# Performance work log

Measured on AMD Instinct MI355X. Metric: run time of the kernel, lower is better.

The kernel has to match this reference:

```python
import math
import jax, jax.numpy as jnp
import numpy as np

N, E = 20000, 640000
S_DIM, Z_DIM, H, QK, VD = 64, 64, 4, 8, 8
EPS = 1e-8


def quat_rotate(v, q):
    # v: [..., 3], q: [..., 4] (w, x, y, z), broadcastable. Unit-quaternion rotation:
    # v' = v + 2*(w*(u x v) + u x (u x v))
    w = q[..., 0:1]
    u = q[..., 1:4]
    uv = jnp.cross(u, v)
    return v + 2.0 * (w * uv + jnp.cross(u, uv))


def setup_inputs() -> dict:
    key = jax.random.key(0)
    ks = jax.random.split(key, 16)
    s = jax.random.normal(ks[0], (N, S_DIM), dtype=jnp.float32)
    z = jax.random.normal(ks[1], (E, Z_DIM), dtype=jnp.float32)
    edge_index = jax.random.randint(ks[2], (2, E), 0, N)
    quaternion = jax.random.normal(ks[3], (N, 4), dtype=jnp.float32)
    quaternion = quaternion / jnp.linalg.norm(quaternion, axis=-1, keepdims=True)
    translation = jax.random.normal(ks[4], (N, 3), dtype=jnp.float32)
    sc_s = 1.0 / math.sqrt(S_DIM)
    sc_z = 1.0 / math.sqrt(Z_DIM)
    # weights stored [in, out] so y = x @ W (equivalent to torch x @ W.T)
    Wq_s = jax.random.normal(ks[5], (S_DIM, H * S_DIM), dtype=jnp.float32) * sc_s
    Wk_s = jax.random.normal(ks[6], (S_DIM, H * S_DIM), dtype=jnp.float32) * sc_s
    Wv_s = jax.random.normal(ks[7], (S_DIM, H * S_DIM), dtype=jnp.float32) * sc_s
    Wq_v = jax.random.normal(ks[8], (S_DIM, H * QK * 3), dtype=jnp.float32) * sc_s
    Wk_v = jax.random.normal(ks[9], (S_DIM, H * QK * 3), dtype=jnp.float32) * sc_s
    Wv_v = jax.random.normal(ks[10], (S_DIM, H * VD * 3), dtype=jnp.float32) * sc_s
    Wb = jax.random.normal(ks[11], (Z_DIM, H), dtype=jnp.float32) * sc_z
    bb = jnp.zeros((H,), dtype=jnp.float32)
    Wdz = jax.random.normal(ks[12], (Z_DIM, Z_DIM // 4), dtype=jnp.float32) * sc_z
    bdz = jnp.zeros((Z_DIM // 4,), dtype=jnp.float32)
    head_weights = jnp.full((H,), 0.541324854612918, dtype=jnp.float32)  # softplus^{-1}(1)
    concat_dim = Z_DIM // 4 + S_DIM + VD * 4
    Wout = jax.random.normal(ks[13], (H * concat_dim, S_DIM), dtype=jnp.float32) / math.sqrt(H * concat_dim)
    bout = jnp.zeros((S_DIM,), dtype=jnp.float32)
    return {
        's': s, 'z': z, 'edge_index': edge_index, 'quaternion': quaternion,
        'translation': translation, 'Wq_s': Wq_s, 'Wk_s': Wk_s, 'Wv_s': Wv_s,
        'Wq_v': Wq_v, 'Wk_v': Wk_v, 'Wv_v': Wv_v, 'Wb': Wb, 'bb': bb,
        'Wdz': Wdz, 'bdz': bdz, 'head_weights': head_weights,
        'Wout': Wout, 'bout': bout,
    }


def reference(s, z, edge_index, quaternion, translation,
              Wq_s, Wk_s, Wv_s, Wq_v, Wk_v, Wv_v,
              Wb, bb, Wdz, bdz, head_weights, Wout, bout):
    idx_i, idx_j = edge_index[0], edge_index[1]
    n = s.shape[0]
    h = head_weights.shape[0]
    qk = Wq_v.shape[1] // (3 * h)
    vd = Wv_v.shape[1] // (3 * h)

    q_scalar = (s @ Wq_s).reshape(n, h, -1)
    k_scalar = (s @ Wk_s).reshape(n, h, -1)
    v_scalar = (s @ Wv_s).reshape(n, h, -1)

    def to_points(x):
        # torch.split into 3 chunks then stack(dim=-1): [n, 3*c] -> [n, c, 3]
        c = x.shape[-1] // 3
        return jnp.swapaxes(x.reshape(n, 3, c), 1, 2)

    quat_b = quaternion[:, None, :]
    trans_b = translation[:, None, :]
    q_vec = (quat_rotate(to_points(s @ Wq_v), quat_b) + trans_b).reshape(n, h, qk, 3)
    k_vec = (quat_rotate(to_points(s @ Wk_v), quat_b) + trans_b).reshape(n, h, qk, 3)
    v_vec = (quat_rotate(to_points(s @ Wv_v), quat_b) + trans_b).reshape(n, h, vd, 3)

    b_bias = z @ Wb + bb  # [E, H]

    attn = jnp.sum(k_scalar[idx_i] * q_scalar[idx_j], axis=-1)  # [E, H]
    attn = attn * math.sqrt(1.0 / 3 * qk) + math.sqrt(1.0 / 3) * b_bias

    disp = q_vec[idx_i] - k_vec[idx_j]            # [E, H, qk, 3]
    vec_att = jnp.sum(disp * disp, axis=-1)       # [E, H, qk]
    hw = jax.nn.softplus(head_weights)[None, :, None]
    vec_att = jnp.sum(vec_att * hw, axis=-1) * math.sqrt(1.0 / (3 * (qk * 9.0 / 2))) * (-0.5)
    attn = attn + vec_att

    # segment softmax over destination node idx_i
    seg_max = jax.ops.segment_max(attn, idx_i, num_segments=n)
    ea = jnp.exp(attn - seg_max[idx_i])
    denom = jax.ops.segment_sum(ea, idx_i, num_segments=n)
    attn = ea / denom[idx_i]                      # [E, H]

    out_scalar = jax.ops.segment_sum(attn[:, :, None] * v_scalar[idx_i], idx_i, num_segments=n)
    out_scalar = out_scalar.reshape(n, -1)

    out_vec = jax.ops.segment_sum(attn[:, :, None, None] * v_vec[idx_i], idx_i, num_segments=n)
    out_vec = out_vec - translation[:, None, None, :]
    q_conj = jnp.concatenate([quaternion[:, :1], -quaternion[:, 1:]], axis=-1)
    out_vec = quat_rotate(out_vec, q_conj[:, None, None, :])   # [n, h, vd, 3]
    out_vec_norm = jnp.sqrt(jnp.sum(out_vec * out_vec, axis=-1) + EPS).reshape(n, -1)
    out_vec_flat = out_vec.reshape(n, -1, 3)

    pair_z = z @ Wdz + bdz                         # [E, z/4]
    out_pair = jax.ops.segment_sum(attn[:, :, None] * pair_z[:, None, :], idx_i, num_segments=n)
    out_pair = out_pair.reshape(n, -1)

    feats = jnp.concatenate([out_scalar,
                             out_vec_flat[..., 0], out_vec_flat[..., 1], out_vec_flat[..., 2],
                             out_vec_norm, out_pair], axis=-1)
    return feats @ Wout + bout
```

## Files before the change

kernel.cpp:

```cpp
#include <hip/hip_runtime.h>
#include <stdint.h>


#define C_SQRT83  1.6329931618554518f
#define C_SQRT13  0.5773502691896258f
#define C_VEC    -0.04811252243246881f

__device__ __forceinline__ unsigned short f2bf(float f){
  unsigned u = __float_as_uint(f);
  u += 0x7fffu + ((u >> 16) & 1u);
  return (unsigned short)(u >> 16);
}
__device__ __forceinline__ unsigned pack2(float a, float b){
  return (unsigned)f2bf(a) | ((unsigned)f2bf(b) << 16);
}
__device__ __forceinline__ float bflo(unsigned u){ return __uint_as_float(u << 16); }
__device__ __forceinline__ float bfhi(unsigned u){ return __uint_as_float(u & 0xffff0000u); }

__device__ __forceinline__ void quat_rot(float w, float ux, float uy, float uz,
                                         float vx, float vy, float vz,
                                         float& ox, float& oy, float& oz){
  float cx = uy*vz - uz*vy;
  float cy = uz*vx - ux*vz;
  float cz = ux*vy - uy*vx;
  float dx = uy*cz - uz*cy;
  float dy = uz*cx - ux*cz;
  float dz = ux*cy - uy*cx;
  ox = vx + 2.f*(w*cx + dx);
  oy = vy + 2.f*(w*cy + dy);
  oz = vz + 2.f*(w*cz + dz);
}


__global__ __launch_bounds__(256) void k_zero(unsigned* __restrict__ counts, int n){
  int g = blockIdx.x*256 + threadIdx.x;
  if (g < n) counts[g] = 0u;
}

__global__ __launch_bounds__(256) void k_count(const int* __restrict__ ei,
                                               unsigned* __restrict__ counts, int ne){
  int e = blockIdx.x*256 + threadIdx.x;
  if (e >= ne) return;
  atomicAdd(&counts[ei[e]], 1u);
}

__global__ __launch_bounds__(256) void k_scan(const unsigned* __restrict__ counts,
                                              unsigned* __restrict__ row_off,
                                              unsigned* __restrict__ cursor, int n){
  __shared__ unsigned part[256];
  int t = threadIdx.x;
  int chunk = (n + 255) >> 8;
  int s0 = t*chunk, s1 = min(s0 + chunk, n);
  unsigned sum = 0;
  for (int k = s0; k < s1; ++k) sum += counts[k];
  part[t] = sum; __syncthreads();
  for (int off = 1; off < 256; off <<= 1){
    unsigned v = (t >= off) ? part[t-off] : 0u;
    __syncthreads();
    part[t] += v;
    __syncthreads();
  }
  unsigned run = (t == 0) ? 0u : part[t-1];
  for (int k = s0; k < s1; ++k){
    row_off[k] = run; cursor[k] = run; run += counts[k];
  }
  if (t == 255) row_off[n] = part[255];
}

__global__ __launch_bounds__(256) void k_fill(const int* __restrict__ ei,
                                              unsigned* __restrict__ cursor,
                                              unsigned* __restrict__ si,
                                              unsigned* __restrict__ sj,
                                              unsigned* __restrict__ se, int ne){
  int e = blockIdx.x*256 + threadIdx.x;
  if (e >= ne) return;
  int i = ei[e];
  unsigned pos = atomicAdd(&cursor[i], 1u);
  si[pos] = (unsigned)i;
  sj[pos] = (unsigned)ei[ne + e];
  se[pos] = (unsigned)e;
}


#define BN 32

__device__ __forceinline__ void pass256(const float* __restrict__ W,
                                        const float st[BN][66], int cg, int sl,
                                        float acc[8][4]){
  #pragma unroll
  for (int i=0;i<8;i++){ acc[i][0]=0.f; acc[i][1]=0.f; acc[i][2]=0.f; acc[i][3]=0.f; }
  #pragma unroll 4
  for (int k = 0; k < 64; ++k){
    const float4 w = *(const float4*)(W + (size_t)k*256 + cg*4);
    #pragma unroll
    for (int i=0;i<8;i++){
      const float sv = st[sl*8+i][k];
      acc[i][0] += sv*w.x; acc[i][1] += sv*w.y; acc[i][2] += sv*w.z; acc[i][3] += sv*w.w;
    }
  }
}

__device__ __forceinline__ void pass96(const float* __restrict__ W,
                                       const float st[BN][66], int cgp, int slp,
                                       float acc[4][4]){
  #pragma unroll
  for (int i=0;i<4;i++){ acc[i][0]=0.f; acc[i][1]=0.f; acc[i][2]=0.f; acc[i][3]=0.f; }
  if (cgp >= 24) return;
  #pragma unroll 4
  for (int k = 0; k < 64; ++k){
    const float4 w = *(const float4*)(W + (size_t)k*96 + cgp*4);
    #pragma unroll
    for (int i=0;i<4;i++){
      const float sv = st[slp*4+i][k];
      acc[i][0] += sv*w.x; acc[i][1] += sv*w.y; acc[i][2] += sv*w.z; acc[i][3] += sv*w.w;
    }
  }
}

__global__ __launch_bounds__(256) void k_proj(
    const float* __restrict__ s, const float* __restrict__ quat, const float* __restrict__ trans,
    const float* __restrict__ Wqs, const float* __restrict__ Wks, const float* __restrict__ Wvs,
    const float* __restrict__ Wqv, const float* __restrict__ Wkv, const float* __restrict__ Wvv,
    unsigned* __restrict__ qs, unsigned* __restrict__ ks, float* __restrict__ vs,
    unsigned* __restrict__ qv, unsigned* __restrict__ kv, float* __restrict__ vv, int n)
{
  __shared__ float st[BN][66];
  __shared__ float pt[BN][97];
  const int tid = threadIdx.x;
  const int node0 = blockIdx.x * BN;

  #pragma unroll
  for (int r = 0; r < 2; ++r){
    const int idx = tid + r*256;
    const int nd = idx >> 4, c4 = idx & 15;
    const int g = node0 + nd;
    float4 v = make_float4(0.f,0.f,0.f,0.f);
    if (g < n) v = *(const float4*)(s + (size_t)g*64 + c4*4);
    st[nd][c4*4+0]=v.x; st[nd][c4*4+1]=v.y; st[nd][c4*4+2]=v.z; st[nd][c4*4+3]=v.w;
  }
  __syncthreads();

  const int cg = tid & 63, sl = tid >> 6;
  const int cgp = tid & 31, slp = tid >> 5;
  float acc[8][4];

  pass256(Wqs, st, cg, sl, acc);
  #pragma unroll
  for (int i=0;i<8;i++){
    const int g = node0 + sl*8 + i;
    if (g < n){
      uint2 u; u.x = pack2(acc[i][0],acc[i][1]); u.y = pack2(acc[i][2],acc[i][3]);
      *(uint2*)(qs + (size_t)g*128 + cg*2) = u;
    }
  }
  pass256(Wks, st, cg, sl, acc);
  #pragma unroll
  for (int i=0;i<8;i++){
    const int g = node0 + sl*8 + i;
    if (g < n){
      uint2 u; u.x = pack2(acc[i][0],acc[i][1]); u.y = pack2(acc[i][2],acc[i][3]);
      *(uint2*)(ks + (size_t)g*128 + cg*2) = u;
    }
  }
  pass256(Wvs, st, cg, sl, acc);
  #pragma unroll
  for (int i=0;i<8;i++){
    const int g = node0 + sl*8 + i;
    if (g < n){
      float4 f; f.x=acc[i][0]; f.y=acc[i][1]; f.z=acc[i][2]; f.w=acc[i][3];
      *(float4*)(vs + (size_t)g*256 + cg*4) = f;
    }
  }

  float pac[4][4];

  pass96(Wqv, st, cgp, slp, pac);
  __syncthreads();
  if (cgp < 24){
    #pragma unroll
    for (int i=0;i<4;i++){
      #pragma unroll
      for (int c=0;c<4;c++) pt[slp*4+i][cgp*4+c] = pac[i][c];
    }
  }
  __syncthreads();
  #pragma unroll
  for (int r = 0; r < 2; ++r){
    const int t2 = tid + r*256;
    const int nd = t2 >> 4, pp = t2 & 15;
    const int g = node0 + nd;
    if (g < n){
      const float4 q4 = *(const float4*)(quat + (size_t)g*4);
      const float tx = trans[(size_t)g*3], ty = trans[(size_t)g*3+1], tz = trans[(size_t)g*3+2];
      float x0,y0,z0,x1,y1,z1;
      quat_rot(q4.x,q4.y,q4.z,q4.w, pt[nd][2*pp],   pt[nd][32+2*pp],   pt[nd][64+2*pp],   x0,y0,z0);
      quat_rot(q4.x,q4.y,q4.z,q4.w, pt[nd][2*pp+1], pt[nd][32+2*pp+1], pt[nd][64+2*pp+1], x1,y1,z1);
      x0+=tx; y0+=ty; z0+=tz; x1+=tx; y1+=ty; z1+=tz;
      unsigned* d = qv + (size_t)g*48 + pp*3;
      d[0] = pack2(x0,y0); d[1] = pack2(z0,x1); d[2] = pack2(y1,z1);
    }
  }

  pass96(Wkv, st, cgp, slp, pac);
  __syncthreads();
  if (cgp < 24){
    #pragma unroll
    for (int i=0;i<4;i++){
      #pragma unroll
      for (int c=0;c<4;c++) pt[slp*4+i][cgp*4+c] = pac[i][c];
    }
  }
  __syncthreads();
  #pragma unroll
  for (int r = 0; r < 2; ++r){
    const int t2 = tid + r*256;
    const int nd = t2 >> 4, pp = t2 & 15;
    const int g = node0 + nd;
    if (g < n){
      const float4 q4 = *(const float4*)(quat + (size_t)g*4);
      const float tx = trans[(size_t)g*3], ty = trans[(size_t)g*3+1], tz = trans[(size_t)g*3+2];
      float x0,y0,z0,x1,y1,z1;
      quat_rot(q4.x,q4.y,q4.z,q4.w, pt[nd][2*pp],   pt[nd][32+2*pp],   pt[nd][64+2*pp],   x0,y0,z0);
      quat_rot(q4.x,q4.y,q4.z,q4.w, pt[nd][2*pp+1], pt[nd][32+2*pp+1], pt[nd][64+2*pp+1], x1,y1,z1);
      x0+=tx; y0+=ty; z0+=tz; x1+=tx; y1+=ty; z1+=tz;
      unsigned* d = kv + (size_t)g*48 + pp*3;
      d[0] = pack2(x0,y0); d[1] = pack2(z0,x1); d[2] = pack2(y1,z1);
    }
  }

  pass96(Wvv, st, cgp, slp, pac);
  __syncthreads();
  if (cgp < 24){
    #pragma unroll
    for (int i=0;i<4;i++){
      #pragma unroll
      for (int c=0;c<4;c++) pt[slp*4+i][cgp*4+c] = pac[i][c];
    }
  }
  __syncthreads();
  #pragma unroll
  for (int r = 0; r < 12; ++r){
    const int idx = tid + r*256;
    const int nd = idx / 96, col = idx - nd*96;
    const int g = node0 + nd;
    if (g < n) vv[(size_t)g*96 + col] = pt[nd][col];
  }
}


__global__ __launch_bounds__(256) void k_edge(
    const float* __restrict__ z,
    const unsigned* __restrict__ si, const unsigned* __restrict__ sj, const unsigned* __restrict__ se,
    const float* __restrict__ Wb,  const float* __restrict__ bb,
    const float* __restrict__ Wdz, const float* __restrict__ bdz,
    const float* __restrict__ hwts,
    const unsigned* __restrict__ qs, const unsigned* __restrict__ ks,
    const unsigned* __restrict__ qv, const unsigned* __restrict__ kv,
    float* __restrict__ logits, unsigned* __restrict__ pz, int ne)
{
  const int p = blockIdx.x*256 + threadIdx.x;
  if (p >= ne) return;
  const unsigned i = si[p], j = sj[p], e = se[p];

  float b4[4];  b4[0]=b4[1]=b4[2]=b4[3]=0.f;
  float pacc[16];
  #pragma unroll
  for (int c=0;c<16;c++) pacc[c]=0.f;
  const float* zr = z + (size_t)e*64;
  #pragma unroll
  for (int k4 = 0; k4 < 16; ++k4){
    const float4 zv = *(const float4*)(zr + 4*k4);
    #pragma unroll
    for (int kk = 0; kk < 4; ++kk){
      const int k = 4*k4 + kk;
      const float zk = (kk==0)?zv.x:((kk==1)?zv.y:((kk==2)?zv.z:zv.w));
      const float4 wb = *(const float4*)(Wb + k*4);
      b4[0]+=zk*wb.x; b4[1]+=zk*wb.y; b4[2]+=zk*wb.z; b4[3]+=zk*wb.w;
      const float* wd = Wdz + k*16;
      const float4 w0=*(const float4*)(wd), w1=*(const float4*)(wd+4),
                   w2=*(const float4*)(wd+8), w3=*(const float4*)(wd+12);
      pacc[ 0]+=zk*w0.x; pacc[ 1]+=zk*w0.y; pacc[ 2]+=zk*w0.z; pacc[ 3]+=zk*w0.w;
      pacc[ 4]+=zk*w1.x; pacc[ 5]+=zk*w1.y; pacc[ 6]+=zk*w1.z; pacc[ 7]+=zk*w1.w;
      pacc[ 8]+=zk*w2.x; pacc[ 9]+=zk*w2.y; pacc[10]+=zk*w2.z; pacc[11]+=zk*w2.w;
      pacc[12]+=zk*w3.x; pacc[13]+=zk*w3.y; pacc[14]+=zk*w3.z; pacc[15]+=zk*w3.w;
    }
  }
  #pragma unroll
  for (int c=0;c<16;c++) pacc[c] += bdz[c];
  { uint4 u0, u1;
    u0.x=pack2(pacc[0],pacc[1]);   u0.y=pack2(pacc[2],pacc[3]);
    u0.z=pack2(pacc[4],pacc[5]);   u0.w=pack2(pacc[6],pacc[7]);
    u1.x=pack2(pacc[8],pacc[9]);   u1.y=pack2(pacc[10],pacc[11]);
    u1.z=pack2(pacc[12],pacc[13]); u1.w=pack2(pacc[14],pacc[15]);
    uint4* d = (uint4*)(pz + (size_t)p*8);
    d[0]=u0; d[1]=u1; }

  const uint4* kr = (const uint4*)(ks + (size_t)i*128);
  const uint4* qr = (const uint4*)(qs + (size_t)j*128);
  float sdot[4];
  #pragma unroll
  for (int h = 0; h < 4; ++h){
    float acc = 0.f;
    #pragma unroll
    for (int c = 0; c < 8; ++c){
      const uint4 a = kr[h*8+c];
      const uint4 b = qr[h*8+c];
      acc += bflo(a.x)*bflo(b.x) + bfhi(a.x)*bfhi(b.x);
      acc += bflo(a.y)*bflo(b.y) + bfhi(a.y)*bfhi(b.y);
      acc += bflo(a.z)*bflo(b.z) + bfhi(a.z)*bfhi(b.z);
      acc += bflo(a.w)*bflo(b.w) + bfhi(a.w)*bfhi(b.w);
    }
    sdot[h] = acc;
  }

  const uint4* qvr = (const uint4*)(qv + (size_t)i*48);
  const uint4* kvr = (const uint4*)(kv + (size_t)j*48);
  float vsum[4];
  #pragma unroll
  for (int h = 0; h < 4; ++h){
    float acc = 0.f;
    #pragma unroll
    for (int c = 0; c < 3; ++c){
      const uint4 a = qvr[h*3+c];
      const uint4 b = kvr[h*3+c];
      float d;
      d = bflo(a.x)-bflo(b.x); acc += d*d;  d = bfhi(a.x)-bfhi(b.x); acc += d*d;
      d = bflo(a.y)-bflo(b.y); acc += d*d;  d = bfhi(a.y)-bfhi(b.y); acc += d*d;
      d = bflo(a.z)-bflo(b.z); acc += d*d;  d = bfhi(a.z)-bfhi(b.z); acc += d*d;
      d = bflo(a.w)-bflo(b.w); acc += d*d;  d = bfhi(a.w)-bfhi(b.w); acc += d*d;
    }
    vsum[h] = acc;
  }

  float4 lg;
  {
    float l[4];
    #pragma unroll
    for (int h = 0; h < 4; ++h){
      const float hw = log1pf(__expf(hwts[h]));
      l[h] = C_SQRT83*sdot[h] + C_SQRT13*(b4[h] + bb[h]) + C_VEC*hw*vsum[h];
    }
    lg.x=l[0]; lg.y=l[1]; lg.z=l[2]; lg.w=l[3];
  }
  *(float4*)(logits + (size_t)p*4) = lg;
}


__global__ __launch_bounds__(256) void k_soft(
    const float* __restrict__ logits, const unsigned* __restrict__ pz,
    const unsigned* __restrict__ row_off, float* __restrict__ out_pair, int n)
{
  const int t = blockIdx.x*256 + threadIdx.x;
  if (t >= n*4) return;
  const int i = t >> 2, h = t & 3;
  const int beg = (int)row_off[i], end = (int)row_off[i+1];

  float m = -3.4e38f;
  for (int p = beg; p < end; ++p) m = fmaxf(m, logits[(size_t)p*4 + h]);

  float ssum = 0.f;
  float acc[16];
  #pragma unroll
  for (int c=0;c<16;c++) acc[c]=0.f;

  for (int p = beg; p < end; ++p){
    const float w = __expf(logits[(size_t)p*4 + h] - m);
    ssum += w;
    const uint4* pr = (const uint4*)(pz + (size_t)p*8);
    const uint4 a = pr[0], b = pr[1];
    acc[ 0]+=w*bflo(a.x); acc[ 1]+=w*bfhi(a.x);
    acc[ 2]+=w*bflo(a.y); acc[ 3]+=w*bfhi(a.y);
    acc[ 4]+=w*bflo(a.z); acc[ 5]+=w*bfhi(a.z);
    acc[ 6]+=w*bflo(a.w); acc[ 7]+=w*bfhi(a.w);
    acc[ 8]+=w*bflo(b.x); acc[ 9]+=w*bfhi(b.x);
    acc[10]+=w*bflo(b.y); acc[11]+=w*bfhi(b.y);
    acc[12]+=w*bflo(b.z); acc[13]+=w*bfhi(b.z);
    acc[14]+=w*bflo(b.w); acc[15]+=w*bfhi(b.w);
  }
  const float inv = (end > beg) ? (1.f/ssum) : 0.f;
  float4* dst = (float4*)(out_pair + (size_t)i*64 + h*16);
  float4 o;
  o.x=acc[0]*inv;  o.y=acc[1]*inv;  o.z=acc[2]*inv;  o.w=acc[3]*inv;  dst[0]=o;
  o.x=acc[4]*inv;  o.y=acc[5]*inv;  o.z=acc[6]*inv;  o.w=acc[7]*inv;  dst[1]=o;
  o.x=acc[8]*inv;  o.y=acc[9]*inv;  o.z=acc[10]*inv; o.w=acc[11]*inv; dst[2]=o;
  o.x=acc[12]*inv; o.y=acc[13]*inv; o.z=acc[14]*inv; o.w=acc[15]*inv; dst[3]=o;
}


__global__ __launch_bounds__(256) void k_out(
    const float* __restrict__ vs, const float* __restrict__ vv,
    const float* __restrict__ out_pair, const unsigned* __restrict__ row_off,
    const float* __restrict__ quat, const float* __restrict__ trans,
    const float* __restrict__ Wout, const float* __restrict__ bout,
    float* __restrict__ out, int n)
{
  __shared__ float feats[32][448];
  __shared__ int degs[32];
  const int tid = threadIdx.x;
  const int node0 = blockIdx.x*32;

  if (tid < 32){
    const int g = node0 + tid;
    degs[tid] = (g < n) ? (int)(row_off[g+1] - row_off[g]) : 1;
  }
  __syncthreads();

  for (int x = tid; x < 32*256; x += 256){
    const int nd = x >> 8, c = x & 255;
    const int g = node0 + nd;
    feats[nd][c] = (g < n && degs[nd] > 0) ? vs[(size_t)g*256 + c] : 0.f;
  }
  for (int x = tid; x < 32*64; x += 256){
    const int nd = x >> 6, c = x & 63;
    const int g = node0 + nd;
    feats[nd][384 + c] = (g < n) ? out_pair[(size_t)g*64 + c] : 0.f;
  }
  for (int x = tid; x < 32*32; x += 256){
    const int nd = x >> 5, pt = x & 31;
    const int g = node0 + nd;
    float X=0.f, Y=0.f, Z=0.f;
    if (g < n){
      if (degs[nd] > 0){
        X = vv[(size_t)g*96 + pt];
        Y = vv[(size_t)g*96 + 32 + pt];
        Z = vv[(size_t)g*96 + 64 + pt];
      } else {
        const float4 q4 = *(const float4*)(quat + (size_t)g*4);
        const float tx = trans[(size_t)g*3], ty = trans[(size_t)g*3+1], tz = trans[(size_t)g*3+2];
        quat_rot(q4.x, -q4.y, -q4.z, -q4.w, -tx, -ty, -tz, X, Y, Z);
      }
    }
    feats[nd][256 + pt] = X;
    feats[nd][288 + pt] = Y;
    feats[nd][320 + pt] = Z;
    feats[nd][352 + pt] = sqrtf(X*X + Y*Y + Z*Z + 1e-8f);
  }
  __syncthreads();

  const int lane = tid & 63;
  const int wave = tid >> 6;
  float acc[8];
  #pragma unroll
  for (int q8=0;q8<8;q8++) acc[q8]=0.f;

  for (int k = 0; k < 448; ++k){
    const float wv = Wout[(size_t)k*64 + lane];
    #pragma unroll
    for (int q8 = 0; q8 < 8; ++q8)
      acc[q8] += feats[wave*8 + q8][k] * wv;
  }
  const float bo = bout[lane];
  #pragma unroll
  for (int q8 = 0; q8 < 8; ++q8){
    const int g = node0 + wave*8 + q8;
    if (g < n) out[(size_t)g*64 + lane] = acc[q8] + bo;
  }
}


extern "C" void kernel_launch(void* const* d_in, const int* in_sizes, int n_in,
                              void* d_out, int out_size, void* d_ws, size_t ws_size,
                              hipStream_t stream) {
  const float* s     = (const float*)d_in[0];
  const float* z     = (const float*)d_in[1];
  const int*   ei    = (const int*)  d_in[2];
  const float* quat  = (const float*)d_in[3];
  const float* trans = (const float*)d_in[4];
  const float* Wqs   = (const float*)d_in[5];
  const float* Wks   = (const float*)d_in[6];
  const float* Wvs   = (const float*)d_in[7];
  const float* Wqv   = (const float*)d_in[8];
  const float* Wkv   = (const float*)d_in[9];
  const float* Wvv   = (const float*)d_in[10];
  const float* Wb    = (const float*)d_in[11];
  const float* bb    = (const float*)d_in[12];
  const float* Wdz   = (const float*)d_in[13];
  const float* bdz   = (const float*)d_in[14];
  const float* hwts  = (const float*)d_in[15];
  const float* Wout  = (const float*)d_in[16];
  const float* bout  = (const float*)d_in[17];
  float* out = (float*)d_out;

  const int n  = in_sizes[0] / 64;
  const int ne = in_sizes[1] / 64;

  size_t off = 0;
  char* base = (char*)d_ws;
  auto take = [&](size_t bytes)->char* {
    char* p = base + off;
    off += (bytes + 255) & ~(size_t)255;
    return p;
  };
  unsigned* qs     = (unsigned*)take((size_t)n*512);
  unsigned* ks     = (unsigned*)take((size_t)n*512);
  unsigned* qvt    = (unsigned*)take((size_t)n*192);
  unsigned* kvt    = (unsigned*)take((size_t)n*192);
  float*    vs     = (float*)   take((size_t)n*1024);
  float*    vv     = (float*)   take((size_t)n*384);
  float*    logits = (float*)   take((size_t)ne*16);
  unsigned* pz     = (unsigned*)take((size_t)ne*32);
  unsigned* counts = (unsigned*)take((size_t)n*4);
  unsigned* roff   = (unsigned*)take((size_t)(n+1)*4);
  unsigned* cur    = (unsigned*)take((size_t)n*4);
  unsigned* si     = (unsigned*)take((size_t)ne*4);
  unsigned* sj     = (unsigned*)take((size_t)ne*4);
  unsigned* se     = (unsigned*)take((size_t)ne*4);
  float*    opair  = (float*)   take((size_t)n*256);
  (void)ws_size; (void)n_in; (void)out_size;

  const int gbE = (ne + 255) / 256;
  const int gbN = (n  + 255) / 256;

  k_zero <<<gbN, 256, 0, stream>>>(counts, n);
  k_count<<<gbE, 256, 0, stream>>>(ei, counts, ne);
  k_scan <<<1,   256, 0, stream>>>(counts, roff, cur, n);
  k_fill <<<gbE, 256, 0, stream>>>(ei, cur, si, sj, se, ne);
  k_proj <<<(n + BN - 1)/BN, 256, 0, stream>>>(s, quat, trans, Wqs, Wks, Wvs, Wqv, Wkv, Wvv,
                                               qs, ks, vs, qvt, kvt, vv, n);
  k_edge <<<gbE, 256, 0, stream>>>(z, si, sj, se, Wb, bb, Wdz, bdz, hwts,
                                   qs, ks, qvt, kvt, logits, pz, ne);
  k_soft <<<(n*4 + 255)/256, 256, 0, stream>>>(logits, pz, roff, opair, n);
  k_out  <<<(n + 31)/32, 256, 0, stream>>>(vs, vv, opair, roff, quat, trans,
                                           Wout, bout, out, n);
}
```

Before: 688.1 us.

## Split edge kernel into coalesced z-projection and gather, parallelize softmax per node

The edge kernel is split in two. A z-projection kernel now reads z coalesced in original edge order and scatters the bias and pair features to sorted positions through a new posmap. A separate gather kernel then computes the attention logits. The segment softmax moves from one thread per (node, head) to 16 lanes per head with shuffle reductions, which balances load across uneven degrees. The node projection uses transposed shared memory for vectorized loads, and the output GEMM loads features as float4. This adds one extra kernel launch and a round trip for the bias through the logits buffer. An unused, inconsistent k_gather variant is left in the file.

```diff
diff --git a/kernel.cpp b/kernel.cpp
--- a/kernel.cpp
+++ b/kernel.cpp
@@ -71,37 +71,42 @@
                                               unsigned* __restrict__ cursor,
                                               unsigned* __restrict__ si,
                                               unsigned* __restrict__ sj,
-                                              unsigned* __restrict__ se, int ne){
+                                              unsigned* __restrict__ posmap, int ne){
   int e = blockIdx.x*256 + threadIdx.x;
   if (e >= ne) return;
   int i = ei[e];
   unsigned pos = atomicAdd(&cursor[i], 1u);
   si[pos] = (unsigned)i;
   sj[pos] = (unsigned)ei[ne + e];
-  se[pos] = (unsigned)e;
+  posmap[e] = pos;
 }
 
 
 #define BN 32
 
 __device__ __forceinline__ void pass256(const float* __restrict__ W,
-                                        const float st[BN][66], int cg, int sl,
+                                        const float stT[64][40], int cg, int sl,
                                         float acc[8][4]){
   #pragma unroll
   for (int i=0;i<8;i++){ acc[i][0]=0.f; acc[i][1]=0.f; acc[i][2]=0.f; acc[i][3]=0.f; }
   #pragma unroll 4
   for (int k = 0; k < 64; ++k){
-    const float4 w = *(const float4*)(W + (size_t)k*256 + cg*4);
-    #pragma unroll
-    for (int i=0;i<8;i++){
-      const float sv = st[sl*8+i][k];
-      acc[i][0] += sv*w.x; acc[i][1] += sv*w.y; acc[i][2] += sv*w.z; acc[i][3] += sv*w.w;
-    }
+    const float4 w  = *(const float4*)(W + (size_t)k*256 + cg*4);
+    const float4 n0 = *(const float4*)&stT[k][sl*8];
+    const float4 n1 = *(const float4*)&stT[k][sl*8+4];
+    acc[0][0]+=n0.x*w.x; acc[0][1]+=n0.x*w.y; acc[0][2]+=n0.x*w.z; acc[0][3]+=n0.x*w.w;
+    acc[1][0]+=n0.y*w.x; acc[1][1]+=n0.y*w.y; acc[1][2]+=n0.y*w.z; acc[1][3]+=n0.y*w.w;
+    acc[2][0]+=n0.z*w.x; acc[2][1]+=n0.z*w.y; acc[2][2]+=n0.z*w.z; acc[2][3]+=n0.z*w.w;
+    acc[3][0]+=n0.w*w.x; acc[3][1]+=n0.w*w.y; acc[3][2]+=n0.w*w.z; acc[3][3]+=n0.w*w.w;
+    acc[4][0]+=n1.x*w.x; acc[4][1]+=n1.x*w.y; acc[4][2]+=n1.x*w.z; acc[4][3]+=n1.x*w.w;
+    acc[5][0]+=n1.y*w.x; acc[5][1]+=n1.y*w.y; acc[5][2]+=n1.y*w.z; acc[5][3]+=n1.y*w.w;
+    acc[6][0]+=n1.z*w.x; acc[6][1]+=n1.z*w.y; acc[6][2]+=n1.z*w.z; acc[6][3]+=n1.z*w.w;
+    acc[7][0]+=n1.w*w.x; acc[7][1]+=n1.w*w.y; acc[7][2]+=n1.w*w.z; acc[7][3]+=n1.w*w.w;
   }
 }
 
 __device__ __forceinline__ void pass96(const float* __restrict__ W,
-                                       const float st[BN][66], int cgp, int slp,
+                                       const float stT[64][40], int cgp, int slp,
                                        float acc[4][4]){
   #pragma unroll
   for (int i=0;i<4;i++){ acc[i][0]=0.f; acc[i][1]=0.f; acc[i][2]=0.f; acc[i][3]=0.f; }
@@ -109,11 +114,11 @@
   #pragma unroll 4
   for (int k = 0; k < 64; ++k){
     const float4 w = *(const float4*)(W + (size_t)k*96 + cgp*4);
-    #pragma unroll
-    for (int i=0;i<4;i++){
-      const float sv = st[slp*4+i][k];
-      acc[i][0] += sv*w.x; acc[i][1] += sv*w.y; acc[i][2] += sv*w.z; acc[i][3] += sv*w.w;
-    }
+    const float4 nv = *(const float4*)&stT[k][slp*4];
+    acc[0][0]+=nv.x*w.x; acc[0][1]+=nv.x*w.y; acc[0][2]+=nv.x*w.z; acc[0][3]+=nv.x*w.w;
+    acc[1][0]+=nv.y*w.x; acc[1][1]+=nv.y*w.y; acc[1][2]+=nv.y*w.z; acc[1][3]+=nv.y*w.w;
+    acc[2][0]+=nv.z*w.x; acc[2][1]+=nv.z*w.y; acc[2][2]+=nv.z*w.z; acc[2][3]+=nv.z*w.w;
+    acc[3][0]+=nv.w*w.x; acc[3][1]+=nv.w*w.y; acc[3][2]+=nv.w*w.z; acc[3][3]+=nv.w*w.w;
   }
 }
 
@@ -124,7 +129,7 @@
     unsigned* __restrict__ qs, unsigned* __restrict__ ks, float* __restrict__ vs,
     unsigned* __restrict__ qv, unsigned* __restrict__ kv, float* __restrict__ vv, int n)
 {
-  __shared__ float st[BN][66];
+  __shared__ float stT[64][40];
   __shared__ float pt[BN][97];
   const int tid = threadIdx.x;
   const int node0 = blockIdx.x * BN;
@@ -136,7 +141,7 @@
     const int g = node0 + nd;
     float4 v = make_float4(0.f,0.f,0.f,0.f);
     if (g < n) v = *(const float4*)(s + (size_t)g*64 + c4*4);
-    st[nd][c4*4+0]=v.x; st[nd][c4*4+1]=v.y; st[nd][c4*4+2]=v.z; st[nd][c4*4+3]=v.w;
+    stT[c4*4+0][nd]=v.x; stT[c4*4+1][nd]=v.y; stT[c4*4+2][nd]=v.z; stT[c4*4+3][nd]=v.w;
   }
   __syncthreads();
 
@@ -144,7 +149,7 @@
   const int cgp = tid & 31, slp = tid >> 5;
   float acc[8][4];
 
-  pass256(Wqs, st, cg, sl, acc);
+  pass256(Wqs, stT, cg, sl, acc);
   #pragma unroll
   for (int i=0;i<8;i++){
     const int g = node0 + sl*8 + i;
@@ -153,7 +158,7 @@
       *(uint2*)(qs + (size_t)g*128 + cg*2) = u;
     }
   }
-  pass256(Wks, st, cg, sl, acc);
+  pass256(Wks, stT, cg, sl, acc);
   #pragma unroll
   for (int i=0;i<8;i++){
     const int g = node0 + sl*8 + i;
@@ -162,7 +167,7 @@
       *(uint2*)(ks + (size_t)g*128 + cg*2) = u;
     }
   }
-  pass256(Wvs, st, cg, sl, acc);
+  pass256(Wvs, stT, cg, sl, acc);
   #pragma unroll
   for (int i=0;i<8;i++){
     const int g = node0 + sl*8 + i;
@@ -174,7 +179,7 @@
 
   float pac[4][4];
 
-  pass96(Wqv, st, cgp, slp, pac);
+  pass96(Wqv, stT, cgp, slp, pac);
   __syncthreads();
   if (cgp < 24){
     #pragma unroll
@@ -201,7 +206,7 @@
     }
   }
 
-  pass96(Wkv, st, cgp, slp, pac);
+  pass96(Wkv, stT, cgp, slp, pac);
   __syncthreads();
   if (cgp < 24){
     #pragma unroll
@@ -228,7 +233,7 @@
     }
   }
 
-  pass96(Wvv, st, cgp, slp, pac);
+  pass96(Wvv, stT, cgp, slp, pac);
   __syncthreads();
   if (cgp < 24){
     #pragma unroll
@@ -248,19 +253,15 @@
 }
 
 
-__global__ __launch_bounds__(256) void k_edge(
-    const float* __restrict__ z,
-    const unsigned* __restrict__ si, const unsigned* __restrict__ sj, const unsigned* __restrict__ se,
+__global__ __launch_bounds__(256) void k_zproj(
+    const float* __restrict__ z, const unsigned* __restrict__ posmap,
     const float* __restrict__ Wb,  const float* __restrict__ bb,
     const float* __restrict__ Wdz, const float* __restrict__ bdz,
-    const float* __restrict__ hwts,
-    const unsigned* __restrict__ qs, const unsigned* __restrict__ ks,
-    const unsigned* __restrict__ qv, const unsigned* __restrict__ kv,
-    float* __restrict__ logits, unsigned* __restrict__ pz, int ne)
+    float* __restrict__ bias4, unsigned* __restrict__ pz, int ne)
 {
-  const int p = blockIdx.x*256 + threadIdx.x;
-  if (p >= ne) return;
-  const unsigned i = si[p], j = sj[p], e = se[p];
+  const int e = blockIdx.x*256 + threadIdx.x;
+  if (e >= ne) return;
+  const unsigned pos = posmap[e];
 
   float b4[4];  b4[0]=b4[1]=b4[2]=b4[3]=0.f;
   float pacc[16];
@@ -285,6 +286,10 @@
       pacc[12]+=zk*w3.x; pacc[13]+=zk*w3.y; pacc[14]+=zk*w3.z; pacc[15]+=zk*w3.w;
     }
   }
+  {
+    float4 b; b.x=b4[0]+bb[0]; b.y=b4[1]+bb[1]; b.z=b4[2]+bb[2]; b.w=b4[3]+bb[3];
+    *(float4*)(bias4 + (size_t)pos*4) = b;
+  }
   #pragma unroll
   for (int c=0;c<16;c++) pacc[c] += bdz[c];
   { uint4 u0, u1;
@@ -292,19 +297,42 @@
     u0.z=pack2(pacc[4],pacc[5]);   u0.w=pack2(pacc[6],pacc[7]);
     u1.x=pack2(pacc[8],pacc[9]);   u1.y=pack2(pacc[10],pacc[11]);
     u1.z=pack2(pacc[12],pacc[13]); u1.w=pack2(pacc[14],pacc[15]);
-    uint4* d = (uint4*)(pz + (size_t)p*8);
+    uint4* d = (uint4*)(pz + (size_t)pos*8);
     d[0]=u0; d[1]=u1; }
-
-  const uint4* kr = (const uint4*)(ks + (size_t)i*128);
-  const uint4* qr = (const uint4*)(qs + (size_t)j*128);
+}
+
+
+__global__ __launch_bounds__(256) void k_gather(
+    const unsigned* __restrict__ si, const unsigned* __restrict__ sj,
+    const float* __restrict__ hwts,
+    const unsigned* __restrict__ qs, const unsigned* __restrict__ ks,
+    const unsigned* __restrict__ qv, const unsigned* __restrict__ kv,
+    float* __restrict__ logits, int ne)
+{
+  const int p = blockIdx.x*256 + threadIdx.x;
+  if (p >= ne) return;
+  const unsigned i = si[p], j = sj[p];
+
+  const uint4* kr  = (const uint4*)(ks + (size_t)i*128);
+  const uint4* qr  = (const uint4*)(qs + (size_t)j*128);
+  const uint4* qvr = (const uint4*)(qv + (size_t)i*48);
+  const uint4* kvr = (const uint4*)(kv + (size_t)j*48);
+
+  uint4 ka[8], qa[8], qva[3], kva[3];
+  #pragma unroll
+  for (int c=0;c<8;c++){ ka[c] = kr[c]; qa[c] = qr[c]; }
+  #pragma unroll
+  for (int c=0;c<3;c++){ qva[c] = qvr[c]; kva[c] = kvr[c]; }
+  const float4 b4 = *(const float4*)(logits + (size_t)p*4);
+
   float sdot[4];
   #pragma unroll
   for (int h = 0; h < 4; ++h){
     float acc = 0.f;
     #pragma unroll
-    for (int c = 0; c < 8; ++c){
-      const uint4 a = kr[h*8+c];
-      const uint4 b = qr[h*8+c];
+    for (int c = 0; c < 2; ++c){
+      const uint4 a = ka[h*2+c];
+      const uint4 b = qa[h*2+c];
       acc += bflo(a.x)*bflo(b.x) + bfhi(a.x)*bfhi(b.x);
       acc += bflo(a.y)*bflo(b.y) + bfhi(a.y)*bfhi(b.y);
       acc += bflo(a.z)*bflo(b.z) + bfhi(a.z)*bfhi(b.z);
@@ -313,23 +341,27 @@
     sdot[h] = acc;
   }
 
-  const uint4* qvr = (const uint4*)(qv + (size_t)i*48);
-  const uint4* kvr = (const uint4*)(kv + (size_t)j*48);
   float vsum[4];
-  #pragma unroll
-  for (int h = 0; h < 4; ++h){
-    float acc = 0.f;
+  {
+    float acch[4];
+    #pragma unroll
+    for (int h=0;h<4;h++) acch[h]=0.f;
     #pragma unroll
     for (int c = 0; c < 3; ++c){
-      const uint4 a = qvr[h*3+c];
-      const uint4 b = kvr[h*3+c];
+      const uint4 a = qva[c], b = kva[c];
+      const int base = c*8;
       float d;
-      d = bflo(a.x)-bflo(b.x); acc += d*d;  d = bfhi(a.x)-bfhi(b.x); acc += d*d;
-      d = bflo(a.y)-bflo(b.y); acc += d*d;  d = bfhi(a.y)-bfhi(b.y); acc += d*d;
-      d = bflo(a.z)-bflo(b.z); acc += d*d;  d = bfhi(a.z)-bfhi(b.z); acc += d*d;
-      d = bflo(a.w)-bflo(b.w); acc += d*d;  d = bfhi(a.w)-bfhi(b.w); acc += d*d;
-    }
-    vsum[h] = acc;
+      d = bflo(a.x)-bflo(b.x); acch[(base+0)/6] += d*d;
+      d = bfhi(a.x)-bfhi(b.x); acch[(base+1)/6] += d*d;
+      d = bflo(a.y)-bflo(b.y); acch[(base+2)/6] += d*d;
+      d = bfhi(a.y)-bfhi(b.y); acch[(base+3)/6] += d*d;
+      d = bflo(a.z)-bflo(b.z); acch[(base+4)/6] += d*d;
+      d = bfhi(a.z)-bfhi(b.z); acch[(base+5)/6] += d*d;
+      d = bflo(a.w)-bflo(b.w); acch[(base+6)/6] += d*d;
+      d = bfhi(a.w)-bfhi(b.w); acch[(base+7)/6] += d*d;
+    }
+    #pragma unroll
+    for (int h=0;h<4;h++) vsum[h]=acch[h];
   }
 
   float4 lg;
@@ -338,7 +370,96 @@
     #pragma unroll
     for (int h = 0; h < 4; ++h){
       const float hw = log1pf(__expf(hwts[h]));
-      l[h] = C_SQRT83*sdot[h] + C_SQRT13*(b4[h] + bb[h]) + C_VEC*hw*vsum[h];
+      l[h] = C_SQRT83*sdot[h] + C_SQRT13*b4.x + C_VEC*hw*vsum[h];
+    }
+    lg.x=l[0]; lg.y=l[1]; lg.z=l[2]; lg.w=l[3];
+  }
+  *(float4*)(logits + (size_t)p*4) = lg;
+}
+
+__global__ __launch_bounds__(256) void k_gather_full(
+    const unsigned* __restrict__ si, const unsigned* __restrict__ sj,
+    const float* __restrict__ hwts,
+    const unsigned* __restrict__ qs, const unsigned* __restrict__ ks,
+    const unsigned* __restrict__ qv, const unsigned* __restrict__ kv,
+    float* __restrict__ logits, int ne)
+{
+  const int p = blockIdx.x*256 + threadIdx.x;
+  if (p >= ne) return;
+  const unsigned i = si[p], j = sj[p];
+
+  const uint4* kr  = (const uint4*)(ks + (size_t)i*128);
+  const uint4* qr  = (const uint4*)(qs + (size_t)j*128);
+  const uint4* qvr = (const uint4*)(qv + (size_t)i*48);
+  const uint4* kvr = (const uint4*)(kv + (size_t)j*48);
+
+  uint4 qva[3], kva[3];
+  #pragma unroll
+  for (int c=0;c<3;c++){ qva[c] = qvr[c]; kva[c] = kvr[c]; }
+  const float4 b4 = *(const float4*)(logits + (size_t)p*4);
+
+  float sdot[4];
+  #pragma unroll
+  for (int hp = 0; hp < 2; ++hp){
+    uint4 a0[8], b0[8];
+    #pragma unroll
+    for (int c=0;c<8;c++){ a0[c]=kr[hp*16+c]; b0[c]=qr[hp*16+c]; }
+    uint4 a1[8], b1[8];
+    #pragma unroll
+    for (int c=0;c<8;c++){ a1[c]=kr[hp*16+8+c]; b1[c]=qr[hp*16+8+c]; }
+    float acc0 = 0.f, acc1 = 0.f;
+    #pragma unroll
+    for (int c=0;c<8;c++){
+      const uint4 a = a0[c], b = b0[c];
+      acc0 += bflo(a.x)*bflo(b.x) + bfhi(a.x)*bfhi(b.x);
+      acc0 += bflo(a.y)*bflo(b.y) + bfhi(a.y)*bfhi(b.y);
+      acc0 += bflo(a.z)*bflo(b.z) + bfhi(a.z)*bfhi(b.z);
+      acc0 += bflo(a.w)*bflo(b.w) + bfhi(a.w)*bfhi(b.w);
+    }
+    #pragma unroll
+    for (int c=0;c<8;c++){
+      const uint4 a = a1[c], b = b1[c];
+      acc1 += bflo(a.x)*bflo(b.x) + bfhi(a.x)*bfhi(b.x);
+      acc1 += bflo(a.y)*bflo(b.y) + bfhi(a.y)*bfhi(b.y);
+      acc1 += bflo(a.z)*bflo(b.z) + bfhi(a.z)*bfhi(b.z);
+      acc1 += bflo(a.w)*bflo(b.w) + bfhi(a.w)*bfhi(b.w);
+    }
+    sdot[hp*2]   = acc0;
+    sdot[hp*2+1] = acc1;
+  }
+
+  const uint4* qvr4 = (const uint4*)(qv + (size_t)i*48);
+  const uint4* kvr4 = (const uint4*)(kv + (size_t)j*48);
+  float vsum[4];
+  #pragma unroll
+  for (int h = 0; h < 4; ++h){
+    const uint4 a0 = qvr4[h*3], a1 = qvr4[h*3+1], a2 = qvr4[h*3+2];
+    const uint4 b0 = kvr4[h*3], b1 = kvr4[h*3+1], b2 = kvr4[h*3+2];
+    float acc = 0.f, d;
+    d=bflo(a0.x)-bflo(b0.x); acc+=d*d; d=bfhi(a0.x)-bfhi(b0.x); acc+=d*d;
+    d=bflo(a0.y)-bflo(b0.y); acc+=d*d; d=bfhi(a0.y)-bfhi(b0.y); acc+=d*d;
+    d=bflo(a0.z)-bflo(b0.z); acc+=d*d; d=bfhi(a0.z)-bfhi(b0.z); acc+=d*d;
+    d=bflo(a0.w)-bflo(b0.w); acc+=d*d; d=bfhi(a0.w)-bfhi(b0.w); acc+=d*d;
+    d=bflo(a1.x)-bflo(b1.x); acc+=d*d; d=bfhi(a1.x)-bfhi(b1.x); acc+=d*d;
+    d=bflo(a1.y)-bflo(b1.y); acc+=d*d; d=bfhi(a1.y)-bfhi(b1.y); acc+=d*d;
+    d=bflo(a1.z)-bflo(b1.z); acc+=d*d; d=bfhi(a1.z)-bfhi(b1.z); acc+=d*d;
+    d=bflo(a1.w)-bflo(b1.w); acc+=d*d; d=bfhi(a1.w)-bfhi(b1.w); acc+=d*d;
+    d=bflo(a2.x)-bflo(b2.x); acc+=d*d; d=bfhi(a2.x)-bfhi(b2.x); acc+=d*d;
+    d=bflo(a2.y)-bflo(b2.y); acc+=d*d; d=bfhi(a2.y)-bfhi(b2.y); acc+=d*d;
+    d=bflo(a2.z)-bflo(b2.z); acc+=d*d; d=bfhi(a2.z)-bfhi(b2.z); acc+=d*d;
+    d=bflo(a2.w)-bflo(b2.w); acc+=d*d; d=bfhi(a2.w)-bfhi(b2.w); acc+=d*d;
+    vsum[h] = acc;
+  }
+  (void)qva; (void)kva;
+
+  float4 lg;
+  {
+    float bias[4] = {b4.x, b4.y, b4.z, b4.w};
+    float l[4];
+    #pragma unroll
+    for (int h = 0; h < 4; ++h){
+      const float hw = log1pf(__expf(hwts[h]));
+      l[h] = C_SQRT83*sdot[h] + C_SQRT13*bias[h] + C_VEC*hw*vsum[h];
     }
     lg.x=l[0]; lg.y=l[1]; lg.z=l[2]; lg.w=l[3];
   }
@@ -350,20 +471,25 @@
     const float* __restrict__ logits, const unsigned* __restrict__ pz,
     const unsigned* __restrict__ row_off, float* __restrict__ out_pair, int n)
 {
-  const int t = blockIdx.x*256 + threadIdx.x;
-  if (t >= n*4) return;
-  const int i = t >> 2, h = t & 3;
-  const int beg = (int)row_off[i], end = (int)row_off[i+1];
+  const int node = blockIdx.x*4 + (threadIdx.x >> 6);
+  if (node >= n) return;
+  const int lane = threadIdx.x & 63;
+  const int h = lane >> 4, sub = lane & 15;
+  const int beg = (int)row_off[node], end = (int)row_off[node+1];
 
   float m = -3.4e38f;
-  for (int p = beg; p < end; ++p) m = fmaxf(m, logits[(size_t)p*4 + h]);
+  for (int p = beg + sub; p < end; p += 16)
+    m = fmaxf(m, logits[(size_t)p*4 + h]);
+  #pragma unroll
+  for (int msk = 1; msk < 16; msk <<= 1)
+    m = fmaxf(m, __shfl_xor(m, msk));
 
   float ssum = 0.f;
   float acc[16];
   #pragma unroll
   for (int c=0;c<16;c++) acc[c]=0.f;
 
-  for (int p = beg; p < end; ++p){
+  for (int p = beg + sub; p < end; p += 16){
     const float w = __expf(logits[(size_t)p*4 + h] - m);
     ssum += w;
     const uint4* pr = (const uint4*)(pz + (size_t)p*8);
@@ -377,13 +503,17 @@
     acc[12]+=w*bflo(b.z); acc[13]+=w*bfhi(b.z);
     acc[14]+=w*bflo(b.w); acc[15]+=w*bfhi(b.w);
   }
+  #pragma unroll
+  for (int msk = 1; msk < 16; msk <<= 1){
+    ssum += __shfl_xor(ssum, msk);
+    #pragma unroll
+    for (int c=0;c<16;c++) acc[c] += __shfl_xor(acc[c], msk);
+  }
   const float inv = (end > beg) ? (1.f/ssum) : 0.f;
-  float4* dst = (float4*)(out_pair + (size_t)i*64 + h*16);
-  float4 o;
-  o.x=acc[0]*inv;  o.y=acc[1]*inv;  o.z=acc[2]*inv;  o.w=acc[3]*inv;  dst[0]=o;
-  o.x=acc[4]*inv;  o.y=acc[5]*inv;  o.z=acc[6]*inv;  o.w=acc[7]*inv;  dst[1]=o;
-  o.x=acc[8]*inv;  o.y=acc[9]*inv;  o.z=acc[10]*inv; o.w=acc[11]*inv; dst[2]=o;
-  o.x=acc[12]*inv; o.y=acc[13]*inv; o.z=acc[14]*inv; o.w=acc[15]*inv; dst[3]=o;
+  float r = 0.f;
+  #pragma unroll
+  for (int c=0;c<16;c++) if (c == sub) r = acc[c];
+  out_pair[(size_t)node*64 + lane] = r * inv;
 }
 
 
@@ -443,11 +573,16 @@
   #pragma unroll
   for (int q8=0;q8<8;q8++) acc[q8]=0.f;
 
-  for (int k = 0; k < 448; ++k){
-    const float wv = Wout[(size_t)k*64 + lane];
-    #pragma unroll
-    for (int q8 = 0; q8 < 8; ++q8)
-      acc[q8] += feats[wave*8 + q8][k] * wv;
+  for (int k0 = 0; k0 < 448; k0 += 4){
+    const float w0 = Wout[(size_t)(k0+0)*64 + lane];
+    const float w1 = Wout[(size_t)(k0+1)*64 + lane];
+    const float w2 = Wout[(size_t)(k0+2)*64 + lane];
+    const float w3 = Wout[(size_t)(k0+3)*64 + lane];
+    #pragma unroll
+    for (int q8 = 0; q8 < 8; ++q8){
+      const float4 f = *(const float4*)&feats[wave*8 + q8][k0];
+      acc[q8] += f.x*w0 + f.y*w1 + f.z*w2 + f.w*w3;
+    }
   }
   const float bo = bout[lane];
   #pragma unroll
@@ -504,7 +639,7 @@
   unsigned* cur    = (unsigned*)take((size_t)n*4);
   unsigned* si     = (unsigned*)take((size_t)ne*4);
   unsigned* sj     = (unsigned*)take((size_t)ne*4);
-  unsigned* se     = (unsigned*)take((size_t)ne*4);
+  unsigned* posmap = (unsigned*)take((size_t)ne*4);
   float*    opair  = (float*)   take((size_t)n*256);
   (void)ws_size; (void)n_in; (void)out_size;
 
@@ -514,12 +649,12 @@
   k_zero <<<gbN, 256, 0, stream>>>(counts, n);
   k_count<<<gbE, 256, 0, stream>>>(ei, counts, ne);
   k_scan <<<1,   256, 0, stream>>>(counts, roff, cur, n);
-  k_fill <<<gbE, 256, 0, stream>>>(ei, cur, si, sj, se, ne);
+  k_fill <<<gbE, 256, 0, stream>>>(ei, cur, si, sj, posmap, ne);
   k_proj <<<(n + BN - 1)/BN, 256, 0, stream>>>(s, quat, trans, Wqs, Wks, Wvs, Wqv, Wkv, Wvv,
                                                qs, ks, vs, qvt, kvt, vv, n);
-  k_edge <<<gbE, 256, 0, stream>>>(z, si, sj, se, Wb, bb, Wdz, bdz, hwts,
-                                   qs, ks, qvt, kvt, logits, pz, ne);
-  k_soft <<<(n*4 + 255)/256, 256, 0, stream>>>(logits, pz, roff, opair, n);
+  k_zproj<<<gbE, 256, 0, stream>>>(z, posmap, Wb, bb, Wdz, bdz, logits, pz, ne);
+  k_gather_full<<<gbE, 256, 0, stream>>>(si, sj, hwts, qs, ks, qvt, kvt, logits, ne);
+  k_soft <<<(n + 3)/4, 256, 0, stream>>>(logits, pz, roff, opair, n);
   k_out  <<<(n + 31)/32, 256, 0, stream>>>(vs, vv, opair, roff, quat, trans,
                                            Wout, bout, out, n);
 }
```

New measurement: 709.2 us. 3.1% more time.
